# Kernel optimization log

Measured on AMD Instinct MI355X. Metric: run time of the kernel, lower is better.

Reference implementation:

```python
import jax, jax.numpy as jnp
import numpy as np

E, H, I, K, BLK = 16, 2048, 2048, 4, 32
ALPHA, LIMIT = 1.702, 7.0
T = 1024


def setup_inputs() -> dict:
    key = jax.random.key(0)
    ks = jax.random.split(key, 12)
    f32 = jnp.float32
    return {
        "hidden_states": jax.random.normal(ks[0], (T, H), f32),
        "router_weight": jax.random.normal(ks[1], (E, H), f32) * 0.02,
        "router_bias": jax.random.normal(ks[2], (E,), f32) * 0.02,
        "gate_blocks": jax.random.normal(ks[3], (E, I, H // BLK, BLK), f32),
        "gate_scales": jax.random.uniform(ks[4], (E, I, H // BLK), f32, 0.01, 0.04),
        "gate_bias": jax.random.normal(ks[5], (E, I), f32) * 0.02,
        "up_blocks": jax.random.normal(ks[6], (E, I, H // BLK, BLK), f32),
        "up_scales": jax.random.uniform(ks[7], (E, I, H // BLK), f32, 0.01, 0.04),
        "up_bias": jax.random.normal(ks[8], (E, I), f32) * 0.02,
        "down_blocks": jax.random.normal(ks[9], (E, H, I // BLK, BLK), f32),
        "down_scales": jax.random.uniform(ks[10], (E, H, I // BLK), f32, 0.01, 0.04),
        "down_bias": jax.random.normal(ks[11], (E, H), f32) * 0.02,
    }


def reference(hidden_states, router_weight, router_bias,
              gate_blocks, gate_scales, gate_bias,
              up_blocks, up_scales, up_bias,
              down_blocks, down_scales, down_bias):
    x = hidden_states.reshape(-1, H)              # [T, H]
    t = x.shape[0]

    # --- router: top-k + softmax over top-k, scattered to dense scores ---
    logits = x @ router_weight.T + router_bias    # [T, E]
    topv, topi = jax.lax.top_k(logits, K)         # [T, K]
    topv = jax.nn.softmax(topv, axis=-1)
    scores = jnp.zeros((t, E), x.dtype).at[jnp.arange(t)[:, None], topi].set(topv)

    # --- inline block (mxfp4-style) dequantization: blocks * per-block scale ---
    gate_w = (gate_blocks * gate_scales[..., None]).reshape(E, I, H)
    up_w = (up_blocks * up_scales[..., None]).reshape(E, I, H)
    down_w = (down_blocks * down_scales[..., None]).reshape(E, H, I)

    # --- GptOss GLU experts ---
    g = jnp.einsum('th,eih->eti', x, gate_w) + gate_bias[:, None, :]   # [E, T, I]
    u = jnp.einsum('th,eih->eti', x, up_w) + up_bias[:, None, :]
    g = jnp.minimum(g, LIMIT)
    u = jnp.clip(u, -LIMIT, LIMIT)
    glu = g * jax.nn.sigmoid(g * ALPHA)
    h = (u + 1.0) * glu                                                # [E, T, I]
    o = jnp.einsum('eti,ehi->eth', h, down_w) + down_bias[:, None, :]  # [E, T, H]

    # --- weighted combine by routing scores (zero for unrouted experts) ---
    out = jnp.einsum('eth,te->th', o, scores)
    return out
```

## Files before the change

kernel.cpp:

```cpp
#include <hip/hip_runtime.h>


#define HD 2048
#define ID 2048
#define NE 16
#define NT 1024
#define NTOPK 4
#define NSLOTS (NT * NTOPK)

typedef unsigned short u16;
typedef __attribute__((ext_vector_type(8))) short short8;
typedef __attribute__((ext_vector_type(4))) float f32x4;

__device__ __forceinline__ float bf2f(u16 v) {
    return __uint_as_float(((unsigned)v) << 16);
}
__device__ __forceinline__ u16 f2bf(float f) {
    unsigned u = __float_as_uint(f);
    return (u16)((u + 0x7fffu + ((u >> 16) & 1u)) >> 16);
}

__global__ void router_kernel(const float* __restrict__ x,
                              const float* __restrict__ rw,
                              const float* __restrict__ rb,
                              u16* __restrict__ xb,
                              int* __restrict__ counts,
                              int* __restrict__ topi,
                              float* __restrict__ topv) {
    const int t = blockIdx.x;
    const int lane = threadIdx.x;

    float xr[32];
#pragma unroll
    for (int j = 0; j < 32; ++j) xr[j] = x[(size_t)t * HD + j * 64 + lane];
#pragma unroll
    for (int j = 0; j < 32; ++j) xb[(size_t)t * HD + j * 64 + lane] = f2bf(xr[j]);

    float lg[NE];
#pragma unroll
    for (int e = 0; e < NE; ++e) {
        const float* w = rw + (size_t)e * HD;
        float s = 0.f;
#pragma unroll
        for (int j = 0; j < 32; ++j) s = fmaf(xr[j], w[j * 64 + lane], s);
        for (int off = 32; off > 0; off >>= 1) s += __shfl_xor(s, off);
        lg[e] = s + rb[e];
    }

    if (lane == 0) {
        unsigned used = 0;
        float sv[NTOPK];
        int si[NTOPK];
#pragma unroll
        for (int k = 0; k < NTOPK; ++k) {
            float best = -1e30f;
            int bi = 0;
#pragma unroll
            for (int e = 0; e < NE; ++e) {
                if (!(used & (1u << e)) && lg[e] > best) { best = lg[e]; bi = e; }
            }
            used |= 1u << bi;
            sv[k] = best;
            si[k] = bi;
        }
        const float mx = sv[0];
        float p[NTOPK], sum = 0.f;
#pragma unroll
        for (int k = 0; k < NTOPK; ++k) { p[k] = __expf(sv[k] - mx); sum += p[k]; }
        const float inv = 1.0f / sum;
#pragma unroll
        for (int k = 0; k < NTOPK; ++k) {
            atomicAdd(&counts[si[k]], 1);
            topi[t * NTOPK + k] = si[k];
            topv[t * NTOPK + k] = p[k] * inv;
        }
    }
}

__global__ void bases_kernel(const int* __restrict__ counts, int* __restrict__ bases) {
    if (threadIdx.x == 0) {
        int acc = 0;
#pragma unroll
        for (int e = 0; e < NE; ++e) { bases[e] = acc; acc += counts[e]; }
    }
}

__global__ void assign_kernel(const int* __restrict__ topi, const float* __restrict__ topv,
                              const int* __restrict__ bases, int* __restrict__ cursor,
                              int* __restrict__ tok_slot, float* __restrict__ wgt_slot) {
    const int t = blockIdx.x * 256 + threadIdx.x;
    if (t < NT) {
#pragma unroll
        for (int k = 0; k < NTOPK; ++k) {
            const int e = topi[t * NTOPK + k];
            const int s = atomicAdd(&cursor[e], 1);
            const int slot = bases[e] + s;
            tok_slot[slot] = t;
            wgt_slot[slot] = topv[t * NTOPK + k];
        }
    }
}

__global__ __launch_bounds__(256, 2) void gu_gemm(
    const u16* __restrict__ xb,
    const float* __restrict__ gate_blocks, const float* __restrict__ gate_scales,
    const float* __restrict__ gate_bias,
    const float* __restrict__ up_blocks, const float* __restrict__ up_scales,
    const float* __restrict__ up_bias,
    const int* __restrict__ counts, const int* __restrict__ bases,
    const int* __restrict__ tok_slot,
    u16* __restrict__ gbuf, u16* __restrict__ ubuf) {
    const int e = blockIdx.z >> 1, mat = blockIdx.z & 1;
    const int n_e = counts[e];
    const int mt = blockIdx.y;
    if (mt * 256 >= n_e) return;
    const int rows = min(256, n_e - mt * 256);
    const int base = bases[e] + mt * 256;
    const float* wb = mat ? up_blocks : gate_blocks;
    const float* wsc = mat ? up_scales : gate_scales;
    const float* wbias = mat ? up_bias : gate_bias;
    u16* outb = mat ? ubuf : gbuf;
    const int n0 = blockIdx.x * 64;

    __shared__ __align__(16) short Bsl[2][8][64][8];

    const int tid = threadIdx.x;
    const int wave = tid >> 6, lane = tid & 63;
    const int lr = lane & 15, kch = lane >> 4;

    const u16* ap[4];
#pragma unroll
    for (int mi = 0; mi < 4; ++mi) {
        const int m = wave * 64 + mi * 16 + lr;
        const int tok = tok_slot[base + min(m, rows - 1)];
        ap[mi] = xb + (size_t)tok * HD + kch * 8;
    }

    const int col = tid & 63, q = tid >> 6;
    const float* bptr = wb + ((size_t)e * ID + n0 + col) * HD + q * 16;
    const float* sptr = wsc + ((size_t)e * ID + n0 + col) * (HD / 32);

    f32x4 acc[4][4];
#pragma unroll
    for (int a = 0; a < 4; ++a)
#pragma unroll
        for (int b = 0; b < 4; ++b) acc[a][b] = (f32x4){0.f, 0.f, 0.f, 0.f};

    float4 br0, br1, br2, br3;
    float sc;
#define LOADB(KB)                                                    \
    {                                                                \
        const float4* p = (const float4*)(bptr + (KB) * 64);         \
        br0 = p[0]; br1 = p[1]; br2 = p[2]; br3 = p[3];              \
        sc = sptr[(KB) * 2 + (q >> 1)];                              \
    }
#define WRITEB(BUF)                                                  \
    {                                                                \
        short8 lo, hi;                                               \
        lo[0] = (short)f2bf(br0.x * sc); lo[1] = (short)f2bf(br0.y * sc); \
        lo[2] = (short)f2bf(br0.z * sc); lo[3] = (short)f2bf(br0.w * sc); \
        lo[4] = (short)f2bf(br1.x * sc); lo[5] = (short)f2bf(br1.y * sc); \
        lo[6] = (short)f2bf(br1.z * sc); lo[7] = (short)f2bf(br1.w * sc); \
        hi[0] = (short)f2bf(br2.x * sc); hi[1] = (short)f2bf(br2.y * sc); \
        hi[2] = (short)f2bf(br2.z * sc); hi[3] = (short)f2bf(br2.w * sc); \
        hi[4] = (short)f2bf(br3.x * sc); hi[5] = (short)f2bf(br3.y * sc); \
        hi[6] = (short)f2bf(br3.z * sc); hi[7] = (short)f2bf(br3.w * sc); \
        *(short8*)&Bsl[BUF][q * 2][col][0] = lo;                     \
        *(short8*)&Bsl[BUF][q * 2 + 1][col][0] = hi;                 \
    }

    LOADB(0);
    WRITEB(0);
    LOADB(1);
    __syncthreads();

    for (int kb = 0; kb < 32; ++kb) {
        short8 a0[4], a1[4];
#pragma unroll
        for (int mi = 0; mi < 4; ++mi) {
            a0[mi] = *(const short8*)(ap[mi] + kb * 64);
            a1[mi] = *(const short8*)(ap[mi] + kb * 64 + 32);
        }
        if (kb + 1 < 32) {
            WRITEB((kb + 1) & 1);
            if (kb + 2 < 32) LOADB(kb + 2);
        }
        const int buf = kb & 1;
        short8 bfv[2][4];
#pragma unroll
        for (int s = 0; s < 2; ++s)
#pragma unroll
            for (int ni = 0; ni < 4; ++ni)
                bfv[s][ni] = *(const short8*)&Bsl[buf][s * 4 + kch][ni * 16 + lr][0];
#pragma unroll
        for (int mi = 0; mi < 4; ++mi)
#pragma unroll
            for (int ni = 0; ni < 4; ++ni)
                acc[mi][ni] = __builtin_amdgcn_mfma_f32_16x16x32_bf16(a0[mi], bfv[0][ni], acc[mi][ni], 0, 0, 0);
#pragma unroll
        for (int mi = 0; mi < 4; ++mi)
#pragma unroll
            for (int ni = 0; ni < 4; ++ni)
                acc[mi][ni] = __builtin_amdgcn_mfma_f32_16x16x32_bf16(a1[mi], bfv[1][ni], acc[mi][ni], 0, 0, 0);
        __syncthreads();
    }
#undef LOADB
#undef WRITEB

    const int qq = lane >> 4;
#pragma unroll
    for (int ni = 0; ni < 4; ++ni) {
        const int colo = n0 + ni * 16 + lr;
        const float bv = wbias[e * ID + colo];
#pragma unroll
        for (int mi = 0; mi < 4; ++mi)
#pragma unroll
            for (int j = 0; j < 4; ++j) {
                const int ml = wave * 64 + mi * 16 + qq * 4 + j;
                if (ml < rows) outb[(size_t)(base + ml) * ID + colo] = f2bf(acc[mi][ni][j] + bv);
            }
    }
}

__global__ void act_kernel(const u16* __restrict__ g, const u16* __restrict__ u,
                           u16* __restrict__ h) {
    const size_t i = (size_t)blockIdx.x * 256 + threadIdx.x;
    const int4 gv = ((const int4*)g)[i];
    const int4 uv = ((const int4*)u)[i];
    const int gi[4] = {gv.x, gv.y, gv.z, gv.w};
    const int ui[4] = {uv.x, uv.y, uv.z, uv.w};
    int hi[4];
#pragma unroll
    for (int c = 0; c < 4; ++c) {
        float res[2];
#pragma unroll
        for (int p = 0; p < 2; ++p) {
            float gg = bf2f((u16)(((unsigned)gi[c] >> (16 * p)) & 0xffffu));
            float uu = bf2f((u16)(((unsigned)ui[c] >> (16 * p)) & 0xffffu));
            gg = fminf(gg, 7.0f);
            uu = fminf(fmaxf(uu, -7.0f), 7.0f);
            const float sig = 1.0f / (1.0f + __expf(-1.702f * gg));
            res[p] = (uu + 1.0f) * (gg * sig);
        }
        hi[c] = (int)((unsigned)f2bf(res[0]) | ((unsigned)f2bf(res[1]) << 16));
    }
    ((int4*)h)[i] = make_int4(hi[0], hi[1], hi[2], hi[3]);
}

__global__ __launch_bounds__(256, 2) void down_gemm(
    const u16* __restrict__ hbuf,
    const float* __restrict__ down_blocks, const float* __restrict__ down_scales,
    const float* __restrict__ down_bias,
    const int* __restrict__ counts, const int* __restrict__ bases,
    const int* __restrict__ tok_slot, const float* __restrict__ wgt_slot,
    float* __restrict__ out) {
    const int e = blockIdx.z;
    const int n_e = counts[e];
    const int mt = blockIdx.y;
    if (mt * 256 >= n_e) return;
    const int rows = min(256, n_e - mt * 256);
    const int base = bases[e] + mt * 256;
    const int n0 = blockIdx.x * 64;

    __shared__ __align__(16) short Bsl[2][8][64][8];

    const int tid = threadIdx.x;
    const int wave = tid >> 6, lane = tid & 63;
    const int lr = lane & 15, kch = lane >> 4;

    const u16* ap[4];
#pragma unroll
    for (int mi = 0; mi < 4; ++mi) {
        const int m = wave * 64 + mi * 16 + lr;
        const int slot = base + min(m, rows - 1);
        ap[mi] = hbuf + (size_t)slot * ID + kch * 8;
    }

    const int col = tid & 63, q = tid >> 6;
    const float* bptr = down_blocks + ((size_t)e * HD + n0 + col) * ID + q * 16;
    const float* sptr = down_scales + ((size_t)e * HD + n0 + col) * (ID / 32);

    f32x4 acc[4][4];
#pragma unroll
    for (int a = 0; a < 4; ++a)
#pragma unroll
        for (int b = 0; b < 4; ++b) acc[a][b] = (f32x4){0.f, 0.f, 0.f, 0.f};

    float4 br0, br1, br2, br3;
    float sc;
#define LOADB(KB)                                                    \
    {                                                                \
        const float4* p = (const float4*)(bptr + (KB) * 64);         \
        br0 = p[0]; br1 = p[1]; br2 = p[2]; br3 = p[3];              \
        sc = sptr[(KB) * 2 + (q >> 1)];                              \
    }
#define WRITEB(BUF)                                                  \
    {                                                                \
        short8 lo, hi;                                               \
        lo[0] = (short)f2bf(br0.x * sc); lo[1] = (short)f2bf(br0.y * sc); \
        lo[2] = (short)f2bf(br0.z * sc); lo[3] = (short)f2bf(br0.w * sc); \
        lo[4] = (short)f2bf(br1.x * sc); lo[5] = (short)f2bf(br1.y * sc); \
        lo[6] = (short)f2bf(br1.z * sc); lo[7] = (short)f2bf(br1.w * sc); \
        hi[0] = (short)f2bf(br2.x * sc); hi[1] = (short)f2bf(br2.y * sc); \
        hi[2] = (short)f2bf(br2.z * sc); hi[3] = (short)f2bf(br2.w * sc); \
        hi[4] = (short)f2bf(br3.x * sc); hi[5] = (short)f2bf(br3.y * sc); \
        hi[6] = (short)f2bf(br3.z * sc); hi[7] = (short)f2bf(br3.w * sc); \
        *(short8*)&Bsl[BUF][q * 2][col][0] = lo;                     \
        *(short8*)&Bsl[BUF][q * 2 + 1][col][0] = hi;                 \
    }

    LOADB(0);
    WRITEB(0);
    LOADB(1);
    __syncthreads();

    for (int kb = 0; kb < 32; ++kb) {
        short8 a0[4], a1[4];
#pragma unroll
        for (int mi = 0; mi < 4; ++mi) {
            a0[mi] = *(const short8*)(ap[mi] + kb * 64);
            a1[mi] = *(const short8*)(ap[mi] + kb * 64 + 32);
        }
        if (kb + 1 < 32) {
            WRITEB((kb + 1) & 1);
            if (kb + 2 < 32) LOADB(kb + 2);
        }
        const int buf = kb & 1;
        short8 bfv[2][4];
#pragma unroll
        for (int s = 0; s < 2; ++s)
#pragma unroll
            for (int ni = 0; ni < 4; ++ni)
                bfv[s][ni] = *(const short8*)&Bsl[buf][s * 4 + kch][ni * 16 + lr][0];
#pragma unroll
        for (int mi = 0; mi < 4; ++mi)
#pragma unroll
            for (int ni = 0; ni < 4; ++ni)
                acc[mi][ni] = __builtin_amdgcn_mfma_f32_16x16x32_bf16(a0[mi], bfv[0][ni], acc[mi][ni], 0, 0, 0);
#pragma unroll
        for (int mi = 0; mi < 4; ++mi)
#pragma unroll
            for (int ni = 0; ni < 4; ++ni)
                acc[mi][ni] = __builtin_amdgcn_mfma_f32_16x16x32_bf16(a1[mi], bfv[1][ni], acc[mi][ni], 0, 0, 0);
        __syncthreads();
    }
#undef LOADB
#undef WRITEB

    const int qq = lane >> 4;
    float bvs[4];
#pragma unroll
    for (int ni = 0; ni < 4; ++ni) bvs[ni] = down_bias[e * HD + n0 + ni * 16 + lr];
#pragma unroll
    for (int mi = 0; mi < 4; ++mi)
#pragma unroll
        for (int j = 0; j < 4; ++j) {
            const int ml = wave * 64 + mi * 16 + qq * 4 + j;
            if (ml >= rows) continue;
            const int slot = base + ml;
            const int tok = tok_slot[slot];
            const float wg = wgt_slot[slot];
            float* orow = out + (size_t)tok * HD;
#pragma unroll
            for (int ni = 0; ni < 4; ++ni)
                atomicAdd(&orow[n0 + ni * 16 + lr], wg * (acc[mi][ni][j] + bvs[ni]));
        }
}

extern "C" void kernel_launch(void* const* d_in, const int* in_sizes, int n_in,
                              void* d_out, int out_size, void* d_ws, size_t ws_size,
                              hipStream_t stream) {
    const float* x           = (const float*)d_in[0];
    const float* rw          = (const float*)d_in[1];
    const float* rb          = (const float*)d_in[2];
    const float* gate_blocks = (const float*)d_in[3];
    const float* gate_scales = (const float*)d_in[4];
    const float* gate_bias   = (const float*)d_in[5];
    const float* up_blocks   = (const float*)d_in[6];
    const float* up_scales   = (const float*)d_in[7];
    const float* up_bias     = (const float*)d_in[8];
    const float* down_blocks = (const float*)d_in[9];
    const float* down_scales = (const float*)d_in[10];
    const float* down_bias   = (const float*)d_in[11];
    float* out = (float*)d_out;

    char* ws = (char*)d_ws;
    u16* xb     = (u16*)ws;
    u16* gbuf   = (u16*)(ws + (4 << 20));
    u16* ubuf   = (u16*)(ws + (20 << 20));
    u16* hbuf   = (u16*)(ws + (36 << 20));
    int* counts = (int*)(ws + (52 << 20));
    int* cursor = counts + 16;
    int* basesp = counts + 32;
    int* topi   = counts + 64;
    float* topv = (float*)(counts + 64 + 4096);
    int* tok_slot = (int*)(counts + 64 + 8192);
    float* wgt_slot = (float*)(counts + 64 + 12288);

    hipMemsetAsync(d_out, 0, (size_t)NT * HD * sizeof(float), stream);
    hipMemsetAsync(counts, 0, 128, stream);

    router_kernel<<<NT, 64, 0, stream>>>(x, rw, rb, xb, counts, topi, topv);
    bases_kernel<<<1, 64, 0, stream>>>(counts, basesp);
    assign_kernel<<<NT / 256, 256, 0, stream>>>(topi, topv, basesp, cursor, tok_slot, wgt_slot);
    gu_gemm<<<dim3(ID / 64, 4, NE * 2), 256, 0, stream>>>(
        xb, gate_blocks, gate_scales, gate_bias, up_blocks, up_scales, up_bias,
        counts, basesp, tok_slot, gbuf, ubuf);
    act_kernel<<<(NSLOTS * ID / 8) / 256, 256, 0, stream>>>(gbuf, ubuf, hbuf);
    down_gemm<<<dim3(HD / 64, 4, NE), 256, 0, stream>>>(
        hbuf, down_blocks, down_scales, down_bias, counts, basesp, tok_slot, wgt_slot, out);
}
```

Measured before the change: 1.282 ms.

## Replace LDS-staged weight tiles with per-wave register loads and dequant in MoE GEMMs

Both expert GEMMs drop the shared-memory double buffer for dequantised weights. Each wave instead loads its fp32 weight fragments and scales straight into registers in MFMA operand layout, dequantises them to bf16 in registers, and runs a two-stage register prefetch over 64 k-steps. This removes the LDS writes and reads and the per-iteration block barriers. In exchange, every wave redundantly loads and converts the same weight tile, multiplying global/L2 traffic and dequant ALU work, and the per-lane weight accesses are less coalesced.

```diff
diff --git a/kernel.cpp b/kernel.cpp
--- a/kernel.cpp
+++ b/kernel.cpp
@@ -100,6 +100,37 @@
         }
     }
 }
+
+
+#define LOADB_(BB, SS, KB)                                               \
+    _Pragma("unroll") for (int ni = 0; ni < 4; ++ni) {                   \
+        const float4* p_ = (const float4*)(bp[ni] + (size_t)(KB) * 32);  \
+        BB[ni][0] = p_[0];                                               \
+        BB[ni][1] = p_[1];                                               \
+        SS[ni] = sp[ni][(KB)];                                           \
+    }
+#define LOADA_(AA, KB)                                                   \
+    _Pragma("unroll") for (int mi = 0; mi < 4; ++mi)                     \
+        AA[mi] = *(const short8*)(ap[mi] + (size_t)(KB) * 32);
+#define DEQ_(BB, SS, BF)                                                 \
+    _Pragma("unroll") for (int ni = 0; ni < 4; ++ni) {                   \
+        const float s_ = SS[ni];                                         \
+        short8 f_;                                                       \
+        f_[0] = (short)f2bf(BB[ni][0].x * s_);                           \
+        f_[1] = (short)f2bf(BB[ni][0].y * s_);                           \
+        f_[2] = (short)f2bf(BB[ni][0].z * s_);                           \
+        f_[3] = (short)f2bf(BB[ni][0].w * s_);                           \
+        f_[4] = (short)f2bf(BB[ni][1].x * s_);                           \
+        f_[5] = (short)f2bf(BB[ni][1].y * s_);                           \
+        f_[6] = (short)f2bf(BB[ni][1].z * s_);                           \
+        f_[7] = (short)f2bf(BB[ni][1].w * s_);                           \
+        BF[ni] = f_;                                                     \
+    }
+#define MFMA16_(AA, BF)                                                  \
+    _Pragma("unroll") for (int mi = 0; mi < 4; ++mi)                     \
+        _Pragma("unroll") for (int ni = 0; ni < 4; ++ni)                 \
+            acc[mi][ni] = __builtin_amdgcn_mfma_f32_16x16x32_bf16(       \
+                AA[mi], BF[ni], acc[mi][ni], 0, 0, 0);
 
 __global__ __launch_bounds__(256, 2) void gu_gemm(
     const u16* __restrict__ xb,
@@ -122,8 +153,6 @@
     u16* outb = mat ? ubuf : gbuf;
     const int n0 = blockIdx.x * 64;
 
-    __shared__ __align__(16) short Bsl[2][8][64][8];
-
     const int tid = threadIdx.x;
     const int wave = tid >> 6, lane = tid & 63;
     const int lr = lane & 15, kch = lane >> 4;
@@ -136,9 +165,14 @@
         ap[mi] = xb + (size_t)tok * HD + kch * 8;
     }
 
-    const int col = tid & 63, q = tid >> 6;
-    const float* bptr = wb + ((size_t)e * ID + n0 + col) * HD + q * 16;
-    const float* sptr = wsc + ((size_t)e * ID + n0 + col) * (HD / 32);
+    const float* bp[4];
+    const float* sp[4];
+#pragma unroll
+    for (int ni = 0; ni < 4; ++ni) {
+        const int col = n0 + ni * 16 + lr;
+        bp[ni] = wb + ((size_t)e * ID + col) * HD + kch * 8;
+        sp[ni] = wsc + ((size_t)e * ID + col) * (HD / 32);
+    }
 
     f32x4 acc[4][4];
 #pragma unroll
@@ -146,66 +180,33 @@
 #pragma unroll
         for (int b = 0; b < 4; ++b) acc[a][b] = (f32x4){0.f, 0.f, 0.f, 0.f};
 
-    float4 br0, br1, br2, br3;
-    float sc;
-#define LOADB(KB)                                                    \
-    {                                                                \
-        const float4* p = (const float4*)(bptr + (KB) * 64);         \
-        br0 = p[0]; br1 = p[1]; br2 = p[2]; br3 = p[3];              \
-        sc = sptr[(KB) * 2 + (q >> 1)];                              \
-    }
-#define WRITEB(BUF)                                                  \
-    {                                                                \
-        short8 lo, hi;                                               \
-        lo[0] = (short)f2bf(br0.x * sc); lo[1] = (short)f2bf(br0.y * sc); \
-        lo[2] = (short)f2bf(br0.z * sc); lo[3] = (short)f2bf(br0.w * sc); \
-        lo[4] = (short)f2bf(br1.x * sc); lo[5] = (short)f2bf(br1.y * sc); \
-        lo[6] = (short)f2bf(br1.z * sc); lo[7] = (short)f2bf(br1.w * sc); \
-        hi[0] = (short)f2bf(br2.x * sc); hi[1] = (short)f2bf(br2.y * sc); \
-        hi[2] = (short)f2bf(br2.z * sc); hi[3] = (short)f2bf(br2.w * sc); \
-        hi[4] = (short)f2bf(br3.x * sc); hi[5] = (short)f2bf(br3.y * sc); \
-        hi[6] = (short)f2bf(br3.z * sc); hi[7] = (short)f2bf(br3.w * sc); \
-        *(short8*)&Bsl[BUF][q * 2][col][0] = lo;                     \
-        *(short8*)&Bsl[BUF][q * 2 + 1][col][0] = hi;                 \
-    }
-
-    LOADB(0);
-    WRITEB(0);
-    LOADB(1);
-    __syncthreads();
-
-    for (int kb = 0; kb < 32; ++kb) {
-        short8 a0[4], a1[4];
-#pragma unroll
-        for (int mi = 0; mi < 4; ++mi) {
-            a0[mi] = *(const short8*)(ap[mi] + kb * 64);
-            a1[mi] = *(const short8*)(ap[mi] + kb * 64 + 32);
-        }
-        if (kb + 1 < 32) {
-            WRITEB((kb + 1) & 1);
-            if (kb + 2 < 32) LOADB(kb + 2);
-        }
-        const int buf = kb & 1;
-        short8 bfv[2][4];
-#pragma unroll
-        for (int s = 0; s < 2; ++s)
-#pragma unroll
-            for (int ni = 0; ni < 4; ++ni)
-                bfv[s][ni] = *(const short8*)&Bsl[buf][s * 4 + kch][ni * 16 + lr][0];
-#pragma unroll
-        for (int mi = 0; mi < 4; ++mi)
-#pragma unroll
-            for (int ni = 0; ni < 4; ++ni)
-                acc[mi][ni] = __builtin_amdgcn_mfma_f32_16x16x32_bf16(a0[mi], bfv[0][ni], acc[mi][ni], 0, 0, 0);
-#pragma unroll
-        for (int mi = 0; mi < 4; ++mi)
-#pragma unroll
-            for (int ni = 0; ni < 4; ++ni)
-                acc[mi][ni] = __builtin_amdgcn_mfma_f32_16x16x32_bf16(a1[mi], bfv[1][ni], acc[mi][ni], 0, 0, 0);
-        __syncthreads();
-    }
-#undef LOADB
-#undef WRITEB
+    float4 B0[4][2], B1[4][2];
+    float S0[4], S1[4];
+    short8 A0[4], A1[4];
+
+    LOADB_(B0, S0, 0);
+    LOADB_(B1, S1, 1);
+    LOADA_(A0, 0);
+    LOADA_(A1, 1);
+
+    for (int kb = 0; kb < 64; kb += 2) {
+        {
+            short8 bf[4];
+            DEQ_(B0, S0, bf);
+            const int nk = (kb + 2 < 64) ? kb + 2 : 63;
+            LOADB_(B0, S0, nk);
+            MFMA16_(A0, bf);
+            LOADA_(A0, nk);
+        }
+        {
+            short8 bg[4];
+            DEQ_(B1, S1, bg);
+            const int nk = (kb + 3 < 64) ? kb + 3 : 63;
+            LOADB_(B1, S1, nk);
+            MFMA16_(A1, bg);
+            LOADA_(A1, nk);
+        }
+    }
 
     const int qq = lane >> 4;
 #pragma unroll
@@ -262,8 +263,6 @@
     const int base = bases[e] + mt * 256;
     const int n0 = blockIdx.x * 64;
 
-    __shared__ __align__(16) short Bsl[2][8][64][8];
-
     const int tid = threadIdx.x;
     const int wave = tid >> 6, lane = tid & 63;
     const int lr = lane & 15, kch = lane >> 4;
@@ -276,9 +275,14 @@
         ap[mi] = hbuf + (size_t)slot * ID + kch * 8;
     }
 
-    const int col = tid & 63, q = tid >> 6;
-    const float* bptr = down_blocks + ((size_t)e * HD + n0 + col) * ID + q * 16;
-    const float* sptr = down_scales + ((size_t)e * HD + n0 + col) * (ID / 32);
+    const float* bp[4];
+    const float* sp[4];
+#pragma unroll
+    for (int ni = 0; ni < 4; ++ni) {
+        const int col = n0 + ni * 16 + lr;
+        bp[ni] = down_blocks + ((size_t)e * HD + col) * ID + kch * 8;
+        sp[ni] = down_scales + ((size_t)e * HD + col) * (ID / 32);
+    }
 
     f32x4 acc[4][4];
 #pragma unroll
@@ -286,66 +290,33 @@
 #pragma unroll
         for (int b = 0; b < 4; ++b) acc[a][b] = (f32x4){0.f, 0.f, 0.f, 0.f};
 
-    float4 br0, br1, br2, br3;
-    float sc;
-#define LOADB(KB)                                                    \
-    {                                                                \
-        const float4* p = (const float4*)(bptr + (KB) * 64);         \
-        br0 = p[0]; br1 = p[1]; br2 = p[2]; br3 = p[3];              \
-        sc = sptr[(KB) * 2 + (q >> 1)];                              \
-    }
-#define WRITEB(BUF)                                                  \
-    {                                                                \
-        short8 lo, hi;                                               \
-        lo[0] = (short)f2bf(br0.x * sc); lo[1] = (short)f2bf(br0.y * sc); \
-        lo[2] = (short)f2bf(br0.z * sc); lo[3] = (short)f2bf(br0.w * sc); \
-        lo[4] = (short)f2bf(br1.x * sc); lo[5] = (short)f2bf(br1.y * sc); \
-        lo[6] = (short)f2bf(br1.z * sc); lo[7] = (short)f2bf(br1.w * sc); \
-        hi[0] = (short)f2bf(br2.x * sc); hi[1] = (short)f2bf(br2.y * sc); \
-        hi[2] = (short)f2bf(br2.z * sc); hi[3] = (short)f2bf(br2.w * sc); \
-        hi[4] = (short)f2bf(br3.x * sc); hi[5] = (short)f2bf(br3.y * sc); \
-        hi[6] = (short)f2bf(br3.z * sc); hi[7] = (short)f2bf(br3.w * sc); \
-        *(short8*)&Bsl[BUF][q * 2][col][0] = lo;                     \
-        *(short8*)&Bsl[BUF][q * 2 + 1][col][0] = hi;                 \
-    }
-
-    LOADB(0);
-    WRITEB(0);
-    LOADB(1);
-    __syncthreads();
-
-    for (int kb = 0; kb < 32; ++kb) {
-        short8 a0[4], a1[4];
-#pragma unroll
-        for (int mi = 0; mi < 4; ++mi) {
-            a0[mi] = *(const short8*)(ap[mi] + kb * 64);
-            a1[mi] = *(const short8*)(ap[mi] + kb * 64 + 32);
-        }
-        if (kb + 1 < 32) {
-            WRITEB((kb + 1) & 1);
-            if (kb + 2 < 32) LOADB(kb + 2);
-        }
-        const int buf = kb & 1;
-        short8 bfv[2][4];
-#pragma unroll
-        for (int s = 0; s < 2; ++s)
-#pragma unroll
-            for (int ni = 0; ni < 4; ++ni)
-                bfv[s][ni] = *(const short8*)&Bsl[buf][s * 4 + kch][ni * 16 + lr][0];
-#pragma unroll
-        for (int mi = 0; mi < 4; ++mi)
-#pragma unroll
-            for (int ni = 0; ni < 4; ++ni)
-                acc[mi][ni] = __builtin_amdgcn_mfma_f32_16x16x32_bf16(a0[mi], bfv[0][ni], acc[mi][ni], 0, 0, 0);
-#pragma unroll
-        for (int mi = 0; mi < 4; ++mi)
-#pragma unroll
-            for (int ni = 0; ni < 4; ++ni)
-                acc[mi][ni] = __builtin_amdgcn_mfma_f32_16x16x32_bf16(a1[mi], bfv[1][ni], acc[mi][ni], 0, 0, 0);
-        __syncthreads();
-    }
-#undef LOADB
-#undef WRITEB
+    float4 B0[4][2], B1[4][2];
+    float S0[4], S1[4];
+    short8 A0[4], A1[4];
+
+    LOADB_(B0, S0, 0);
+    LOADB_(B1, S1, 1);
+    LOADA_(A0, 0);
+    LOADA_(A1, 1);
+
+    for (int kb = 0; kb < 64; kb += 2) {
+        {
+            short8 bf[4];
+            DEQ_(B0, S0, bf);
+            const int nk = (kb + 2 < 64) ? kb + 2 : 63;
+            LOADB_(B0, S0, nk);
+            MFMA16_(A0, bf);
+            LOADA_(A0, nk);
+        }
+        {
+            short8 bg[4];
+            DEQ_(B1, S1, bg);
+            const int nk = (kb + 3 < 64) ? kb + 3 : 63;
+            LOADB_(B1, S1, nk);
+            MFMA16_(A1, bg);
+            LOADA_(A1, nk);
+        }
+    }
 
     const int qq = lane >> 4;
     float bvs[4];
```

Result: slower. 2.748 ms (+114.3%).
